# Kernel optimization log

Hardware: AMD Instinct MI355X
Metric: run time of the kernel (lower is better)

## Reference

```python
import jax, jax.numpy as jnp
import numpy as np

D = 2048; Nl = 2; Nh = 32; Nkv = 8; V = 32000; Dh = 5632; Lm = 4096
B = 1; L = 2048; E = 1e-5
DHEAD = D // Nh  # 64


def setup_inputs() -> dict:
    key = jax.random.key(0)
    ks = jax.random.split(key, 10)
    s = 0.02
    rn = lambda k, shape: jax.random.normal(k, shape, jnp.float32) * s
    emb = rn(ks[0], (V, D))
    wq = rn(ks[1], (Nl, D, D))
    wk = rn(ks[2], (Nl, D, D * Nkv // Nh))
    wv = rn(ks[3], (Nl, D, D * Nkv // Nh))
    wa = rn(ks[4], (Nl, D, D))
    wg = rn(ks[5], (Nl, D, Dh))
    wu = rn(ks[6], (Nl, D, Dh))
    wd = rn(ks[7], (Nl, Dh, D))
    w_an = jnp.ones((Nl, D), jnp.float32)
    w_fn = jnp.ones((Nl, D), jnp.float32)
    w_on = jnp.ones((D,), jnp.float32)
    w_out = rn(ks[8], (D, V))
    # RoPE tables (interleaved-pair convention, matching reshape(..., -1, 2))
    theta = 1.0 / (10000.0 ** (jnp.arange(0, DHEAD, 2, dtype=jnp.float32) / DHEAD))
    freqs = jnp.outer(jnp.arange(Lm, dtype=jnp.float32), theta)  # [Lm, DHEAD//2]
    cos = jnp.cos(freqs)
    sin = jnp.sin(freqs)
    ti = jax.random.randint(ks[9], (B, L), 0, V)
    return dict(ti=ti, emb=emb, wq=wq, wk=wk, wv=wv, wa=wa, w_an=w_an, w_fn=w_fn,
                wg=wg, wu=wu, wd=wd, w_on=w_on, w_out=w_out, cos=cos, sin=sin)


def _rmsnorm(x, w):
    return x * jax.lax.rsqrt(jnp.mean(x * x, -1, keepdims=True) + E) * w


def _rope(x, cos, sin):
    # x: [B, L, H, DHEAD]; cos/sin: [1, L, 1, DHEAD//2]; interleaved pairs
    xs = x.reshape(*x.shape[:-1], DHEAD // 2, 2)
    xr, xi = xs[..., 0], xs[..., 1]
    r1 = xr * cos - xi * sin
    i1 = xr * sin + xi * cos
    return jnp.stack([r1, i1], axis=-1).reshape(x.shape)


def reference(ti, emb, wq, wk, wv, wa, w_an, w_fn, wg, wu, wd, w_on, w_out, cos, sin):
    cos_l = cos[:L].reshape(1, L, 1, DHEAD // 2)
    sin_l = sin[:L].reshape(1, L, 1, DHEAD // 2)
    mask = jnp.triu(jnp.full((1, 1, L, L), -jnp.inf, jnp.float32), 1)
    scale = 1.0 / jnp.sqrt(jnp.float32(DHEAD))
    rep = Nh // Nkv
    x = emb[ti]  # [B, L, D]
    for l in range(Nl):
        h = _rmsnorm(x, w_an[l])
        q = (h @ wq[l]).reshape(B, L, Nh, DHEAD)
        k = (h @ wk[l]).reshape(B, L, Nkv, DHEAD)
        v = (h @ wv[l]).reshape(B, L, Nkv, DHEAD)
        q = _rope(q, cos_l, sin_l)
        k = _rope(k, cos_l, sin_l)
        kx = jnp.repeat(k, rep, axis=2)  # GQA expand -> [B, L, Nh, DHEAD]
        vx = jnp.repeat(v, rep, axis=2)
        a = jnp.einsum('blhd,bmhd->bhlm', q, kx) * scale
        p = jax.nn.softmax(a + mask, axis=-1)
        sa = jnp.einsum('bhlm,bmhd->blhd', p, vx).reshape(B, L, D)
        x = x + sa @ wa[l]
        hf = _rmsnorm(x, w_fn[l])
        x = x + (jax.nn.silu(hf @ wg[l]) * (hf @ wu[l])) @ wd[l]
    return _rmsnorm(x, w_on) @ w_out  # [B, L, V]
```

## Files before the change

### kernel.cpp

```cpp
#include <hip/hip_runtime.h>
#include <hip/hip_bf16.h>

#define DMODEL 2048
#define LSEQ   2048
#define NHEAD  32
#define NKVH   8
#define DHEAD  64
#define DFF    5632
#define VOCAB  32000

typedef __attribute__((ext_vector_type(8))) short bf16x8;
typedef __attribute__((ext_vector_type(4))) float f32x4;
typedef __attribute__((ext_vector_type(8))) unsigned short ushort8;

__device__ __forceinline__ void gload_lds16(const __hip_bfloat16* g, __hip_bfloat16* l) {
  __builtin_amdgcn_global_load_lds((const void __attribute__((address_space(1)))*)g,
                                   (void __attribute__((address_space(3)))*)l, 16, 0, 0);
}

__device__ __forceinline__ float bfbits2f(unsigned short u) {
  return __uint_as_float(((unsigned int)u) << 16);
}
__device__ __forceinline__ unsigned short f2bfbits(float f) {
  unsigned int x = __float_as_uint(f);
  return (unsigned short)((x + 0x7fffu + ((x >> 16) & 1u)) >> 16);
}

__global__ __launch_bounds__(256) void embed_k(const int* __restrict__ ti,
                                               const float* __restrict__ emb,
                                               float* __restrict__ x) {
  const int row = blockIdx.x;
  const int t = threadIdx.x;
  const int tok = ti[row];
  const float4* s = (const float4*)(emb + (size_t)tok * DMODEL);
  float4* d = (float4*)(x + (size_t)row * DMODEL);
  d[t] = s[t];
  d[t + 256] = s[t + 256];
}

__global__ __launch_bounds__(256) void rmsnorm_k(const float* __restrict__ x,
                                                 const float* __restrict__ w,
                                                 __hip_bfloat16* __restrict__ out) {
  const int row = blockIdx.x;
  const int t = threadIdx.x;
  const float4* xr = (const float4*)(x + (size_t)row * DMODEL);
  float4 a = xr[t];
  float4 b = xr[t + 256];
  float ss = a.x*a.x + a.y*a.y + a.z*a.z + a.w*a.w
           + b.x*b.x + b.y*b.y + b.z*b.z + b.w*b.w;
  #pragma unroll
  for (int m = 32; m >= 1; m >>= 1) ss += __shfl_xor(ss, m);
  __shared__ float red[4];
  if ((t & 63) == 0) red[t >> 6] = ss;
  __syncthreads();
  const float tot = red[0] + red[1] + red[2] + red[3];
  const float sc = rsqrtf(tot * (1.0f / DMODEL) + 1e-5f);
  const float4* w4 = (const float4*)w;
  float4 wa_ = w4[t], wb_ = w4[t + 256];
  __hip_bfloat16* o = out + (size_t)row * DMODEL;
  o[4*t + 0] = __float2bfloat16(a.x * sc * wa_.x);
  o[4*t + 1] = __float2bfloat16(a.y * sc * wa_.y);
  o[4*t + 2] = __float2bfloat16(a.z * sc * wa_.z);
  o[4*t + 3] = __float2bfloat16(a.w * sc * wa_.w);
  o[1024 + 4*t + 0] = __float2bfloat16(b.x * sc * wb_.x);
  o[1024 + 4*t + 1] = __float2bfloat16(b.y * sc * wb_.y);
  o[1024 + 4*t + 2] = __float2bfloat16(b.z * sc * wb_.z);
  o[1024 + 4*t + 3] = __float2bfloat16(b.w * sc * wb_.w);
}

__device__ __forceinline__ void transpose_tile(const float* __restrict__ src,
                                               __hip_bfloat16* __restrict__ dst,
                                               int K, int N, int rstride, int roff,
                                               int kb, int nb, int t) {
  __shared__ float tile[64 * 65];
  #pragma unroll
  for (int i = 0; i < 4; ++i) {
    const int idx = t + 256 * i;
    const int r = idx >> 4;
    const int c4 = (idx & 15) << 2;
    const float4 v = *(const float4*)&src[(size_t)(kb + r) * N + nb + c4];
    tile[r * 65 + c4 + 0] = v.x;
    tile[r * 65 + c4 + 1] = v.y;
    tile[r * 65 + c4 + 2] = v.z;
    tile[r * 65 + c4 + 3] = v.w;
  }
  __syncthreads();
  #pragma unroll
  for (int i = 0; i < 4; ++i) {
    const int idx = t + 256 * i;
    const int n = idx >> 4;
    const int k4 = (idx & 15) << 2;
    ushort4 o;
    o.x = f2bfbits(tile[(k4 + 0) * 65 + n]);
    o.y = f2bfbits(tile[(k4 + 1) * 65 + n]);
    o.z = f2bfbits(tile[(k4 + 2) * 65 + n]);
    o.w = f2bfbits(tile[(k4 + 3) * 65 + n]);
    *(ushort4*)&dst[((size_t)(nb + n) * rstride + roff) * K + kb + k4] = o;
  }
}

__global__ __launch_bounds__(256) void transpose_k(const float* __restrict__ src,
                                                   __hip_bfloat16* __restrict__ dst,
                                                   int K, int N, int rstride, int roff) {
  transpose_tile(src, dst, K, N, rstride, roff, blockIdx.x * 64, blockIdx.y * 64, threadIdx.x);
}

struct TDesc { const float* src; __hip_bfloat16* dst; int K, N, rstride, roff, ntiles, nty; };
struct TBatch { TDesc d[7]; };

__global__ __launch_bounds__(256) void transpose_batch_k(TBatch tb) {
  int bt = blockIdx.x;
  int seg = 0;
  while (seg < 6 && bt >= tb.d[seg].ntiles) { bt -= tb.d[seg].ntiles; ++seg; }
  const TDesc D = tb.d[seg];
  const int kb = (bt / D.nty) * 64;
  const int nb = (bt % D.nty) * 64;
  transpose_tile(D.src, D.dst, D.K, D.N, D.rstride, D.roff, kb, nb, threadIdx.x);
}

template <int EPI>
__global__ __launch_bounds__(256) void gemm_bt(const __hip_bfloat16* __restrict__ A,
                                               const __hip_bfloat16* __restrict__ Bt,
                                               float* __restrict__ Cf,
                                               __hip_bfloat16* __restrict__ Cb,
                                               int M, int N, int K,
                                               const float* __restrict__ cosT = nullptr,
                                               const float* __restrict__ sinT = nullptr) {
  __shared__ __align__(16) __hip_bfloat16 As[128 * 64];
  __shared__ __align__(16) __hip_bfloat16 Bs[128 * 64];
  const int tid = threadIdx.x;
  const int wave = tid >> 6;
  const int lane = tid & 63;
  const int nbx = M >> 7;
  const int nwg = nbx * (N >> 7);
  const int orig = blockIdx.y * nbx + blockIdx.x;
  const int wid = (orig & 7) * (nwg >> 3) + (orig >> 3);
  const int tm = (wid % nbx) << 7;
  const int tn = (wid / nbx) << 7;
  const int wr = (wave >> 1) * 64;
  const int wc = (wave & 1) * 64;
  const int fr = lane & 15;
  const int fg = lane >> 4;
  const int r8 = lane >> 3;
  const int gsrc = ((lane & 7) ^ r8) << 3;
  const int fr7 = fr & 7;
  const f32x4 fzero = {0.f, 0.f, 0.f, 0.f};
  f32x4 acc[4][4];
  #pragma unroll
  for (int i = 0; i < 4; ++i)
    #pragma unroll
    for (int j = 0; j < 4; ++j) acc[i][j] = fzero;
  const __hip_bfloat16* gA = A + (size_t)(tm + wave * 32 + r8) * K + gsrc;
  const __hip_bfloat16* gB = Bt + (size_t)(tn + wave * 32 + r8) * K + gsrc;
  const int c0 = ((0 + fg) ^ fr7) << 3;
  const int c1 = ((4 + fg) ^ fr7) << 3;
  for (int k0 = 0; k0 < K; k0 += 64) {
    #pragma unroll
    for (int j = 0; j < 4; ++j) {
      gload_lds16(gA + (size_t)(j * 8) * K, &As[(wave * 32 + j * 8) * 64]);
      gload_lds16(gB + (size_t)(j * 8) * K, &Bs[(wave * 32 + j * 8) * 64]);
    }
    gA += 64; gB += 64;
    __syncthreads();
    bf16x8 af[4][2], bfr[4][2];
    #pragma unroll
    for (int i = 0; i < 4; ++i) {
      af[i][0] = *(const bf16x8*)&As[(wr + i * 16 + fr) * 64 + c0];
      af[i][1] = *(const bf16x8*)&As[(wr + i * 16 + fr) * 64 + c1];
    }
    #pragma unroll
    for (int j = 0; j < 4; ++j) {
      bfr[j][0] = *(const bf16x8*)&Bs[(wc + j * 16 + fr) * 64 + c0];
      bfr[j][1] = *(const bf16x8*)&Bs[(wc + j * 16 + fr) * 64 + c1];
    }
    #pragma unroll
    for (int ks = 0; ks < 2; ++ks)
      #pragma unroll
      for (int i = 0; i < 4; ++i)
        #pragma unroll
        for (int j = 0; j < 4; ++j)
          acc[i][j] = __builtin_amdgcn_mfma_f32_16x16x32_bf16(af[i][ks], bfr[j][ks], acc[i][j], 0, 0, 0);
    __syncthreads();
  }
  #pragma unroll
  for (int i = 0; i < 4; ++i)
    #pragma unroll
    for (int j = 0; j < 4; ++j)
      #pragma unroll
      for (int r = 0; r < 4; ++r) {
        const int row = tm + wr + i * 16 + fg * 4 + r;
        const int col = tn + wc + j * 16 + fr;
        const float v = acc[i][j][r];
        if (EPI == 0) Cf[(size_t)row * N + col] = v;
        else if (EPI == 1) Cb[(size_t)row * N + col] = __float2bfloat16(v);
        else if (EPI == 2) Cf[(size_t)row * N + col] += v;
        else if (EPI == 4) {
          const float pv = __shfl_xor(v, 1);
          float ov = v;
          if (col < 2560) {
            const int ri = (col & 63) >> 1;
            const float c = cosT[row * 32 + ri];
            const float s = sinT[row * 32 + ri];
            ov = (fr & 1) ? (pv * s + v * c) : (v * c - pv * s);
          }
          Cb[(size_t)row * N + col] = __float2bfloat16(ov);
        }
      }
}

template <int EPI>
__global__ __launch_bounds__(512, 2) void gemm8p(const __hip_bfloat16* __restrict__ A,
                                                 const __hip_bfloat16* __restrict__ Bt,
                                                 float* __restrict__ Cf,
                                                 __hip_bfloat16* __restrict__ Cb,
                                                 int M, int N, int K) {
  __shared__ __align__(16) __hip_bfloat16 lds[2][2][256 * 64];
  const int tid = threadIdx.x;
  const int wave = tid >> 6;
  const int lane = tid & 63;
  const int nbx = M >> 8;
  const int nwg = nbx * (N >> 8);
  const int orig = blockIdx.y * nbx + blockIdx.x;
  const int wid = (orig & 7) * (nwg >> 3) + (orig >> 3);
  const int tm = (wid % nbx) << 8;
  const int tn = (wid / nbx) << 8;
  const int wm = wave >> 2;
  const int wn = wave & 3;
  const int fr = lane & 15;
  const int fg = lane >> 4;
  const int l3 = lane >> 3;
  const int l7 = lane & 7;
  const int swzcol = (l3 ^ l7) << 3;
  const size_t sK = (size_t)K;

  const __hip_bfloat16* pA = A + (size_t)(tm + wave * 8 + l3) * sK + swzcol;
  const __hip_bfloat16* pB = Bt + (size_t)(tn + wave * 8 + l3) * sK + swzcol;

  #pragma unroll
  for (int j = 0; j < 4; ++j) {
    gload_lds16(pA + (size_t)(j * 64) * sK, &lds[0][0][(j * 64 + wave * 8) * 64]);
    gload_lds16(pB + (size_t)(j * 64) * sK, &lds[0][1][(j * 64 + wave * 8) * 64]);
  }
  pA += 64; pB += 64;
  #pragma unroll
  for (int j = 0; j < 4; ++j) {
    gload_lds16(pA + (size_t)(j * 64) * sK, &lds[1][0][(j * 64 + wave * 8) * 64]);
    gload_lds16(pB + (size_t)(j * 64) * sK, &lds[1][1][(j * 64 + wave * 8) * 64]);
  }
  pA += 64; pB += 64;

  const f32x4 fzero = {0.f, 0.f, 0.f, 0.f};
  f32x4 acc[8][4];
  #pragma unroll
  for (int i = 0; i < 8; ++i)
    #pragma unroll
    for (int j = 0; j < 4; ++j) acc[i][j] = fzero;

  const int wmo = wm * 128;
  const int wno = wn * 64;
  const int rswz = (fr & 7) << 4;
  const int ct0 = ((fg * 16) ^ rswz) >> 1;
  const int ct1 = ((64 + fg * 16) ^ rswz) >> 1;

  asm volatile("s_waitcnt vmcnt(8)" ::: "memory");
  __builtin_amdgcn_s_barrier();
  __builtin_amdgcn_sched_barrier(0);

  const int NT = K >> 6;
  for (int kt = 0; kt < NT; ++kt) {
    const int cur = kt & 1;
    const __hip_bfloat16* LA = &lds[cur][0][0];
    const __hip_bfloat16* LB = &lds[cur][1][0];
    bf16x8 av[8][2], bv[4][2];
    #pragma unroll
    for (int mi = 0; mi < 8; ++mi) {
      av[mi][0] = *(const bf16x8*)&LA[(wmo + mi * 16 + fr) * 64 + ct0];
      av[mi][1] = *(const bf16x8*)&LA[(wmo + mi * 16 + fr) * 64 + ct1];
    }
    #pragma unroll
    for (int ni = 0; ni < 4; ++ni) {
      bv[ni][0] = *(const bf16x8*)&LB[(wno + ni * 16 + fr) * 64 + ct0];
      bv[ni][1] = *(const bf16x8*)&LB[(wno + ni * 16 + fr) * 64 + ct1];
    }
    asm volatile("s_waitcnt lgkmcnt(0)" ::: "memory");
    __builtin_amdgcn_sched_barrier(0);
    __builtin_amdgcn_s_barrier();
    __builtin_amdgcn_sched_barrier(0);
    const bool pre = (kt + 2 < NT);
    #pragma unroll
    for (int q = 0; q < 4; ++q) {
      if (pre) {
        gload_lds16(pA + (size_t)(q * 64) * sK, &lds[cur][0][(q * 64 + wave * 8) * 64]);
        gload_lds16(pB + (size_t)(q * 64) * sK, &lds[cur][1][(q * 64 + wave * 8) * 64]);
      }
      const int mb = (q & 1) * 4;
      const int nb = (q >> 1) * 2;
      __builtin_amdgcn_s_setprio(1);
      #pragma unroll
      for (int ks = 0; ks < 2; ++ks)
        #pragma unroll
        for (int mi = 0; mi < 4; ++mi)
          #pragma unroll
          for (int ni = 0; ni < 2; ++ni)
            acc[mb + mi][nb + ni] = __builtin_amdgcn_mfma_f32_16x16x32_bf16(
                av[mb + mi][ks], bv[nb + ni][ks], acc[mb + mi][nb + ni], 0, 0, 0);
      __builtin_amdgcn_s_setprio(0);
    }
    if (pre) { pA += 64; pB += 64; }
    if (kt + 1 < NT) {
      if (pre) asm volatile("s_waitcnt vmcnt(8)" ::: "memory");
      else     asm volatile("s_waitcnt vmcnt(0)" ::: "memory");
      __builtin_amdgcn_s_barrier();
      __builtin_amdgcn_sched_barrier(0);
    }
  }
  #pragma unroll
  for (int mf = 0; mf < 8; ++mf)
    #pragma unroll
    for (int nf = 0; nf < 4; ++nf)
      #pragma unroll
      for (int r = 0; r < 4; ++r) {
        const int row = tm + wmo + mf * 16 + fg * 4 + r;
        const int col = tn + wno + nf * 16 + fr;
        const float v = acc[mf][nf][r];
        if (EPI == 0) Cf[(size_t)row * N + col] = v;
        else if (EPI == 1) Cb[(size_t)row * N + col] = __float2bfloat16(v);
        else if (EPI == 3) {
          const float p = __shfl_xor(v, 1);
          if (!(fr & 1)) {
            const float sv = v / (1.f + __expf(-v)) * p;
            Cb[(size_t)row * (N >> 1) + ((tn + wno + nf * 16) >> 1) + (fr >> 1)] =
                __float2bfloat16(sv);
          }
        }
      }
}

__global__ __launch_bounds__(256) void attn_k(const __hip_bfloat16* __restrict__ qkv,
                                              __hip_bfloat16* __restrict__ out) {
  const int h = blockIdx.x;
  const int qt = 31 - blockIdx.y;
  const int tid = threadIdx.x;
  const int wave = tid >> 6;
  const int lane = tid & 63;
  const int fr = lane & 15;
  const int fg = lane >> 4;
  const int qb = qt * 64;
  const int kcol = DMODEL + (h >> 2) * DHEAD;
  const int vcol = DMODEL + NKVH * DHEAD + (h >> 2) * DHEAD;
  __shared__ __align__(16) __hip_bfloat16 Ks[64 * 64];
  __shared__ __align__(16) __hip_bfloat16 Vt[64 * 72];
  __shared__ __align__(16) __hip_bfloat16 Ps[4][16 * 72];
  bf16x8 qf[2];
  {
    const __hip_bfloat16* qp = qkv + (size_t)(qb + wave * 16 + fr) * 3072 + h * DHEAD + fg * 8;
    qf[0] = *(const bf16x8*)qp;
    qf[1] = *(const bf16x8*)(qp + 32);
  }
  const f32x4 fzero = {0.f, 0.f, 0.f, 0.f};
  float m_run = -1e30f, l_run = 0.f;
  f32x4 o[4];
  #pragma unroll
  for (int c = 0; c < 4; ++c) o[c] = fzero;

  const int kr8 = lane >> 3;
  const int kgr = ((lane & 7) ^ kr8) << 3;
  const int vpr = tid >> 3;
  const int vg = tid & 7;
  const int myq = qb + wave * 16 + fr;
  const int fr7 = fr & 7;

  for (int t = 0; t <= qt; ++t) {
    {
      const __hip_bfloat16* kp = qkv + (size_t)(t * 64 + wave * 16 + kr8) * 3072 + kcol + kgr;
      gload_lds16(kp, &Ks[(wave * 16) * 64]);
      gload_lds16(kp + (size_t)8 * 3072, &Ks[(wave * 16 + 8) * 64]);
    }
    {
      const __hip_bfloat16* vp0 = qkv + (size_t)(t * 64 + 2 * vpr) * 3072 + vcol + vg * 8;
      ushort8 va = *(const ushort8*)vp0;
      ushort8 vb = *(const ushort8*)(vp0 + 3072);
      unsigned short* vt = (unsigned short*)Vt;
      #pragma unroll
      for (int i = 0; i < 8; ++i) {
        unsigned int pk = (unsigned int)va[i] | ((unsigned int)vb[i] << 16);
        *(unsigned int*)(vt + (vg * 8 + i) * 72 + 2 * vpr) = pk;
      }
    }
    __syncthreads();
    f32x4 s[4];
    #pragma unroll
    for (int c = 0; c < 4; ++c) s[c] = fzero;
    #pragma unroll
    for (int ks = 0; ks < 2; ++ks)
      #pragma unroll
      for (int c = 0; c < 4; ++c) {
        bf16x8 kf = *(const bf16x8*)&Ks[(c * 16 + fr) * 64 + (((ks * 4 + fg) ^ fr7) << 3)];
        s[c] = __builtin_amdgcn_mfma_f32_16x16x32_bf16(kf, qf[ks], s[c], 0, 0, 0);
      }
    float pm = -1e30f;
    #pragma unroll
    for (int c = 0; c < 4; ++c)
      #pragma unroll
      for (int r = 0; r < 4; ++r) {
        float v = s[c][r] * 0.125f;
        if (t * 64 + c * 16 + fg * 4 + r > myq) v = -1e30f;
        s[c][r] = v;
        pm = fmaxf(pm, v);
      }
    pm = fmaxf(pm, __shfl_xor(pm, 16));
    pm = fmaxf(pm, __shfl_xor(pm, 32));
    const float mn = fmaxf(m_run, pm);
    const float al = __expf(m_run - mn);
    m_run = mn;
    float rs = 0.f;
    #pragma unroll
    for (int c = 0; c < 4; ++c)
      #pragma unroll
      for (int r = 0; r < 4; ++r) {
        float p = __expf(s[c][r] - mn);
        s[c][r] = p;
        rs += p;
      }
    rs += __shfl_xor(rs, 16);
    rs += __shfl_xor(rs, 32);
    l_run = l_run * al + rs;
    float als[4];
    #pragma unroll
    for (int r = 0; r < 4; ++r) als[r] = __shfl(al, fg * 4 + r);
    #pragma unroll
    for (int c = 0; c < 4; ++c)
      #pragma unroll
      for (int r = 0; r < 4; ++r) o[c][r] *= als[r];
    {
      unsigned short* pw = (unsigned short*)Ps[wave];
      #pragma unroll
      for (int c = 0; c < 4; ++c) {
        unsigned int lo = (unsigned int)f2bfbits(s[c][0]) | ((unsigned int)f2bfbits(s[c][1]) << 16);
        unsigned int hi = (unsigned int)f2bfbits(s[c][2]) | ((unsigned int)f2bfbits(s[c][3]) << 16);
        uint2 pk; pk.x = lo; pk.y = hi;
        *(uint2*)(pw + fr * 72 + c * 16 + fg * 4) = pk;
      }
    }
    #pragma unroll
    for (int ks = 0; ks < 2; ++ks) {
      bf16x8 pf = *(const bf16x8*)&Ps[wave][fr * 72 + ks * 32 + fg * 8];
      #pragma unroll
      for (int c = 0; c < 4; ++c) {
        bf16x8 vf = *(const bf16x8*)&Vt[(c * 16 + fr) * 72 + ks * 32 + fg * 8];
        o[c] = __builtin_amdgcn_mfma_f32_16x16x32_bf16(pf, vf, o[c], 0, 0, 0);
      }
    }
    __syncthreads();
  }
  float lq[4];
  #pragma unroll
  for (int r = 0; r < 4; ++r) lq[r] = __shfl(l_run, fg * 4 + r);
  #pragma unroll
  for (int c = 0; c < 4; ++c)
    #pragma unroll
    for (int r = 0; r < 4; ++r)
      out[(size_t)(qb + wave * 16 + fg * 4 + r) * DMODEL + h * DHEAD + c * 16 + fr] =
          __float2bfloat16(o[c][r] / lq[r]);
}

extern "C" void kernel_launch(void* const* d_in, const int* in_sizes, int n_in,
                              void* d_out, int out_size, void* d_ws, size_t ws_size,
                              hipStream_t stream) {
  const int* ti = (const int*)d_in[0];
  const float* emb = (const float*)d_in[1];
  const float* wq = (const float*)d_in[2];
  const float* wk = (const float*)d_in[3];
  const float* wv = (const float*)d_in[4];
  const float* wa = (const float*)d_in[5];
  const float* w_an = (const float*)d_in[6];
  const float* w_fn = (const float*)d_in[7];
  const float* wg = (const float*)d_in[8];
  const float* wu = (const float*)d_in[9];
  const float* wd = (const float*)d_in[10];
  const float* w_on = (const float*)d_in[11];
  const float* w_out = (const float*)d_in[12];
  const float* cosT = (const float*)d_in[13];
  const float* sinT = (const float*)d_in[14];
  float* outp = (float*)d_out;

  char* ws = (char*)d_ws;
  float* x            = (float*)(ws + 0);
  __hip_bfloat16* h   = (__hip_bfloat16*)(ws + 16777216);
  __hip_bfloat16* qkv = (__hip_bfloat16*)(ws + 25165824);
  __hip_bfloat16* att = (__hip_bfloat16*)(ws + 37748736);
  __hip_bfloat16* mb  = (__hip_bfloat16*)(ws + 92274688);
  __hip_bfloat16* wTqkv = (__hip_bfloat16*)(ws + 115343360);
  __hip_bfloat16* wTa   = (__hip_bfloat16*)(ws + 127926272);
  __hip_bfloat16* wTgu  = (__hip_bfloat16*)(ws + 136314880);
  __hip_bfloat16* wTd   = (__hip_bfloat16*)(ws + 182452224);
  __hip_bfloat16* wTout = (__hip_bfloat16*)(ws + 25165824);
  (void)in_sizes; (void)n_in; (void)out_size; (void)ws_size;

  const dim3 blk(256);
  embed_k<<<2048, blk, 0, stream>>>(ti, emb, x);
  for (int l = 0; l < 2; ++l) {
    TBatch tb;
    tb.d[0] = { wq + (size_t)l * 2048 * 2048, wTqkv,                          2048, 2048, 1, 0, 32 * 32, 32 };
    tb.d[1] = { wk + (size_t)l * 2048 * 512,  wTqkv + (size_t)2048 * 2048,    2048, 512,  1, 0, 32 * 8,  8  };
    tb.d[2] = { wv + (size_t)l * 2048 * 512,  wTqkv + (size_t)2560 * 2048,    2048, 512,  1, 0, 32 * 8,  8  };
    tb.d[3] = { wa + (size_t)l * 2048 * 2048, wTa,                            2048, 2048, 1, 0, 32 * 32, 32 };
    tb.d[4] = { wg + (size_t)l * 2048 * 5632, wTgu,                           2048, 5632, 2, 0, 32 * 88, 88 };
    tb.d[5] = { wu + (size_t)l * 2048 * 5632, wTgu,                           2048, 5632, 2, 1, 32 * 88, 88 };
    tb.d[6] = { wd + (size_t)l * 5632 * 2048, wTd,                            5632, 2048, 1, 0, 88 * 32, 32 };
    const int ntt = 1024 + 256 + 256 + 1024 + 2816 + 2816 + 2816;
    transpose_batch_k<<<ntt, blk, 0, stream>>>(tb);

    rmsnorm_k<<<2048, blk, 0, stream>>>(x, w_an + l * 2048, h);
    gemm_bt<4><<<dim3(16, 24), blk, 0, stream>>>(h, wTqkv, nullptr, qkv, 2048, 3072, 2048, cosT, sinT);
    attn_k<<<dim3(32, 32), blk, 0, stream>>>(qkv, att);
    gemm_bt<2><<<dim3(16, 16), blk, 0, stream>>>(att, wTa, x, nullptr, 2048, 2048, 2048);

    rmsnorm_k<<<2048, blk, 0, stream>>>(x, w_fn + l * 2048, h);
    gemm8p<3><<<dim3(8, 44), dim3(512), 0, stream>>>(h, wTgu, nullptr, mb, 2048, 11264, 2048);
    gemm_bt<2><<<dim3(16, 16), blk, 0, stream>>>(mb, wTd, x, nullptr, 2048, 2048, 5632);
  }
  transpose_k<<<dim3(32, 500), blk, 0, stream>>>(w_out, wTout, 2048, 32000, 1, 0);
  rmsnorm_k<<<2048, blk, 0, stream>>>(x, w_on, h);
  gemm8p<0><<<dim3(8, 125), dim3(512), 0, stream>>>(h, wTout, outp, nullptr, 2048, 32000, 2048);
}
```

Baseline: 1.282 ms.

## Double attention query tile per block and move gate/up GEMM to gemm_bt

The attention kernel now processes 128 query rows per block, two 16-row sub-blocks per wave, so each K/V tile loaded into LDS is reused across twice as many queries and the grid is halved. The fused SiLU-gate epilogue moves from the 8-wave gemm8p kernel into the 256-thread gemm_bt kernel, and the gate/up projection now launches gemm_bt with smaller tiles. The attention change cuts K/V load traffic but raises register pressure and leaves fewer blocks for causal load balancing. The GEMM swap trades the pipelined large-tile kernel for more, smaller blocks.

```diff
diff --git a/kernel.cpp b/kernel.cpp
--- a/kernel.cpp
+++ b/kernel.cpp
@@ -194,7 +194,14 @@
         if (EPI == 0) Cf[(size_t)row * N + col] = v;
         else if (EPI == 1) Cb[(size_t)row * N + col] = __float2bfloat16(v);
         else if (EPI == 2) Cf[(size_t)row * N + col] += v;
-        else if (EPI == 4) {
+        else if (EPI == 3) {
+          const float p = __shfl_xor(v, 1);
+          if (!(fr & 1)) {
+            const float sv = v / (1.f + __expf(-v)) * p;
+            Cb[(size_t)row * (N >> 1) + ((tn + wc + j * 16) >> 1) + (fr >> 1)] =
+                __float2bfloat16(sv);
+          }
+        } else if (EPI == 4) {
           const float pv = __shfl_xor(v, 1);
           float ov = v;
           if (col < 2560) {
@@ -324,53 +331,49 @@
         const int col = tn + wno + nf * 16 + fr;
         const float v = acc[mf][nf][r];
         if (EPI == 0) Cf[(size_t)row * N + col] = v;
-        else if (EPI == 1) Cb[(size_t)row * N + col] = __float2bfloat16(v);
-        else if (EPI == 3) {
-          const float p = __shfl_xor(v, 1);
-          if (!(fr & 1)) {
-            const float sv = v / (1.f + __expf(-v)) * p;
-            Cb[(size_t)row * (N >> 1) + ((tn + wno + nf * 16) >> 1) + (fr >> 1)] =
-                __float2bfloat16(sv);
-          }
-        }
+        else Cb[(size_t)row * N + col] = __float2bfloat16(v);
       }
 }
 
 __global__ __launch_bounds__(256) void attn_k(const __hip_bfloat16* __restrict__ qkv,
                                               __hip_bfloat16* __restrict__ out) {
   const int h = blockIdx.x;
-  const int qt = 31 - blockIdx.y;
+  const int qt = 15 - blockIdx.y;
   const int tid = threadIdx.x;
   const int wave = tid >> 6;
   const int lane = tid & 63;
   const int fr = lane & 15;
   const int fg = lane >> 4;
-  const int qb = qt * 64;
+  const int qb = qt * 128;
   const int kcol = DMODEL + (h >> 2) * DHEAD;
   const int vcol = DMODEL + NKVH * DHEAD + (h >> 2) * DHEAD;
   __shared__ __align__(16) __hip_bfloat16 Ks[64 * 64];
   __shared__ __align__(16) __hip_bfloat16 Vt[64 * 72];
-  __shared__ __align__(16) __hip_bfloat16 Ps[4][16 * 72];
-  bf16x8 qf[2];
-  {
-    const __hip_bfloat16* qp = qkv + (size_t)(qb + wave * 16 + fr) * 3072 + h * DHEAD + fg * 8;
-    qf[0] = *(const bf16x8*)qp;
-    qf[1] = *(const bf16x8*)(qp + 32);
+  __shared__ __align__(16) __hip_bfloat16 Ps[4][32 * 72];
+  bf16x8 qf[2][2];
+  #pragma unroll
+  for (int rb = 0; rb < 2; ++rb) {
+    const __hip_bfloat16* qp =
+        qkv + (size_t)(qb + wave * 32 + rb * 16 + fr) * 3072 + h * DHEAD + fg * 8;
+    qf[rb][0] = *(const bf16x8*)qp;
+    qf[rb][1] = *(const bf16x8*)(qp + 32);
   }
   const f32x4 fzero = {0.f, 0.f, 0.f, 0.f};
-  float m_run = -1e30f, l_run = 0.f;
-  f32x4 o[4];
-  #pragma unroll
-  for (int c = 0; c < 4; ++c) o[c] = fzero;
+  float m_run[2] = {-1e30f, -1e30f}, l_run[2] = {0.f, 0.f};
+  f32x4 o[2][4];
+  #pragma unroll
+  for (int rb = 0; rb < 2; ++rb)
+    #pragma unroll
+    for (int c = 0; c < 4; ++c) o[rb][c] = fzero;
 
   const int kr8 = lane >> 3;
   const int kgr = ((lane & 7) ^ kr8) << 3;
   const int vpr = tid >> 3;
   const int vg = tid & 7;
-  const int myq = qb + wave * 16 + fr;
   const int fr7 = fr & 7;
 
-  for (int t = 0; t <= qt; ++t) {
+  const int NT = 2 * qt + 2;
+  for (int t = 0; t < NT; ++t) {
     {
       const __hip_bfloat16* kp = qkv + (size_t)(t * 64 + wave * 16 + kr8) * 3072 + kcol + kgr;
       gload_lds16(kp, &Ks[(wave * 16) * 64]);
@@ -388,80 +391,87 @@
       }
     }
     __syncthreads();
-    f32x4 s[4];
-    #pragma unroll
-    for (int c = 0; c < 4; ++c) s[c] = fzero;
-    #pragma unroll
-    for (int ks = 0; ks < 2; ++ks)
-      #pragma unroll
-      for (int c = 0; c < 4; ++c) {
-        bf16x8 kf = *(const bf16x8*)&Ks[(c * 16 + fr) * 64 + (((ks * 4 + fg) ^ fr7) << 3)];
-        s[c] = __builtin_amdgcn_mfma_f32_16x16x32_bf16(kf, qf[ks], s[c], 0, 0, 0);
-      }
-    float pm = -1e30f;
-    #pragma unroll
-    for (int c = 0; c < 4; ++c)
-      #pragma unroll
-      for (int r = 0; r < 4; ++r) {
-        float v = s[c][r] * 0.125f;
-        if (t * 64 + c * 16 + fg * 4 + r > myq) v = -1e30f;
-        s[c][r] = v;
-        pm = fmaxf(pm, v);
-      }
-    pm = fmaxf(pm, __shfl_xor(pm, 16));
-    pm = fmaxf(pm, __shfl_xor(pm, 32));
-    const float mn = fmaxf(m_run, pm);
-    const float al = __expf(m_run - mn);
-    m_run = mn;
-    float rs = 0.f;
-    #pragma unroll
-    for (int c = 0; c < 4; ++c)
-      #pragma unroll
-      for (int r = 0; r < 4; ++r) {
-        float p = __expf(s[c][r] - mn);
-        s[c][r] = p;
-        rs += p;
-      }
-    rs += __shfl_xor(rs, 16);
-    rs += __shfl_xor(rs, 32);
-    l_run = l_run * al + rs;
-    float als[4];
-    #pragma unroll
-    for (int r = 0; r < 4; ++r) als[r] = __shfl(al, fg * 4 + r);
-    #pragma unroll
-    for (int c = 0; c < 4; ++c)
-      #pragma unroll
-      for (int r = 0; r < 4; ++r) o[c][r] *= als[r];
-    {
+    #pragma unroll
+    for (int rb = 0; rb < 2; ++rb) {
+      const int myq = qb + wave * 32 + rb * 16 + fr;
+      f32x4 s[4];
+      #pragma unroll
+      for (int c = 0; c < 4; ++c) s[c] = fzero;
+      #pragma unroll
+      for (int ks = 0; ks < 2; ++ks)
+        #pragma unroll
+        for (int c = 0; c < 4; ++c) {
+          bf16x8 kf = *(const bf16x8*)&Ks[(c * 16 + fr) * 64 + (((ks * 4 + fg) ^ fr7) << 3)];
+          s[c] = __builtin_amdgcn_mfma_f32_16x16x32_bf16(kf, qf[rb][ks], s[c], 0, 0, 0);
+        }
+      float pm = -1e30f;
+      #pragma unroll
+      for (int c = 0; c < 4; ++c)
+        #pragma unroll
+        for (int r = 0; r < 4; ++r) {
+          float v = s[c][r] * 0.125f;
+          if (t * 64 + c * 16 + fg * 4 + r > myq) v = -1e30f;
+          s[c][r] = v;
+          pm = fmaxf(pm, v);
+        }
+      pm = fmaxf(pm, __shfl_xor(pm, 16));
+      pm = fmaxf(pm, __shfl_xor(pm, 32));
+      const float mn = fmaxf(m_run[rb], pm);
+      const float al = __expf(m_run[rb] - mn);
+      m_run[rb] = mn;
+      float rs = 0.f;
+      #pragma unroll
+      for (int c = 0; c < 4; ++c)
+        #pragma unroll
+        for (int r = 0; r < 4; ++r) {
+          float p = __expf(s[c][r] - mn);
+          s[c][r] = p;
+          rs += p;
+        }
+      rs += __shfl_xor(rs, 16);
+      rs += __shfl_xor(rs, 32);
+      l_run[rb] = l_run[rb] * al + rs;
+      float als[4];
+      #pragma unroll
+      for (int r = 0; r < 4; ++r) als[r] = __shfl(al, fg * 4 + r);
+      #pragma unroll
+      for (int c = 0; c < 4; ++c)
+        #pragma unroll
+        for (int r = 0; r < 4; ++r) o[rb][c][r] *= als[r];
       unsigned short* pw = (unsigned short*)Ps[wave];
       #pragma unroll
       for (int c = 0; c < 4; ++c) {
         unsigned int lo = (unsigned int)f2bfbits(s[c][0]) | ((unsigned int)f2bfbits(s[c][1]) << 16);
         unsigned int hi = (unsigned int)f2bfbits(s[c][2]) | ((unsigned int)f2bfbits(s[c][3]) << 16);
         uint2 pk; pk.x = lo; pk.y = hi;
-        *(uint2*)(pw + fr * 72 + c * 16 + fg * 4) = pk;
+        *(uint2*)(pw + (rb * 16 + fr) * 72 + c * 16 + fg * 4) = pk;
       }
     }
     #pragma unroll
     for (int ks = 0; ks < 2; ++ks) {
-      bf16x8 pf = *(const bf16x8*)&Ps[wave][fr * 72 + ks * 32 + fg * 8];
+      bf16x8 pf0 = *(const bf16x8*)&Ps[wave][(fr) * 72 + ks * 32 + fg * 8];
+      bf16x8 pf1 = *(const bf16x8*)&Ps[wave][(16 + fr) * 72 + ks * 32 + fg * 8];
       #pragma unroll
       for (int c = 0; c < 4; ++c) {
         bf16x8 vf = *(const bf16x8*)&Vt[(c * 16 + fr) * 72 + ks * 32 + fg * 8];
-        o[c] = __builtin_amdgcn_mfma_f32_16x16x32_bf16(pf, vf, o[c], 0, 0, 0);
+        o[0][c] = __builtin_amdgcn_mfma_f32_16x16x32_bf16(pf0, vf, o[0][c], 0, 0, 0);
+        o[1][c] = __builtin_amdgcn_mfma_f32_16x16x32_bf16(pf1, vf, o[1][c], 0, 0, 0);
       }
     }
     __syncthreads();
   }
-  float lq[4];
-  #pragma unroll
-  for (int r = 0; r < 4; ++r) lq[r] = __shfl(l_run, fg * 4 + r);
-  #pragma unroll
-  for (int c = 0; c < 4; ++c)
-    #pragma unroll
-    for (int r = 0; r < 4; ++r)
-      out[(size_t)(qb + wave * 16 + fg * 4 + r) * DMODEL + h * DHEAD + c * 16 + fr] =
-          __float2bfloat16(o[c][r] / lq[r]);
+  #pragma unroll
+  for (int rb = 0; rb < 2; ++rb) {
+    float lq[4];
+    #pragma unroll
+    for (int r = 0; r < 4; ++r) lq[r] = __shfl(l_run[rb], fg * 4 + r);
+    #pragma unroll
+    for (int c = 0; c < 4; ++c)
+      #pragma unroll
+      for (int r = 0; r < 4; ++r)
+        out[(size_t)(qb + wave * 32 + rb * 16 + fg * 4 + r) * DMODEL + h * DHEAD + c * 16 + fr] =
+            __float2bfloat16(o[rb][c][r] / lq[r]);
+  }
 }
 
 extern "C" void kernel_launch(void* const* d_in, const int* in_sizes, int n_in,
@@ -513,11 +523,11 @@
 
     rmsnorm_k<<<2048, blk, 0, stream>>>(x, w_an + l * 2048, h);
     gemm_bt<4><<<dim3(16, 24), blk, 0, stream>>>(h, wTqkv, nullptr, qkv, 2048, 3072, 2048, cosT, sinT);
-    attn_k<<<dim3(32, 32), blk, 0, stream>>>(qkv, att);
+    attn_k<<<dim3(32, 16), blk, 0, stream>>>(qkv, att);
     gemm_bt<2><<<dim3(16, 16), blk, 0, stream>>>(att, wTa, x, nullptr, 2048, 2048, 2048);
 
     rmsnorm_k<<<2048, blk, 0, stream>>>(x, w_fn + l * 2048, h);
-    gemm8p<3><<<dim3(8, 44), dim3(512), 0, stream>>>(h, wTgu, nullptr, mb, 2048, 11264, 2048);
+    gemm_bt<3><<<dim3(16, 88), blk, 0, stream>>>(h, wTgu, nullptr, mb, 2048, 11264, 2048);
     gemm_bt<2><<<dim3(16, 16), blk, 0, stream>>>(mb, wTd, x, nullptr, 2048, 2048, 5632);
   }
   transpose_k<<<dim3(32, 500), blk, 0, stream>>>(w_out, wTout, 2048, 32000, 1, 0);
```

After: 1.315 ms. +2.6%, slower.
